# Performance work log

Hardware: AMD Instinct MI355X
Metric: run time of the kernel (lower is better)

Reference implementation:

```python
import jax, jax.numpy as jnp
import numpy as np

EMBED_DIM = 1024
VOCAB = 32000
B, S = 4, 4096


def setup_inputs() -> dict:
    key = jax.random.key(0)
    ks = jax.random.split(key, 6)
    scale = 1.0 / np.sqrt(EMBED_DIM)
    x = jax.random.randint(ks[0], (B, S), 0, VOCAB, dtype=jnp.int64)
    embed = jax.random.normal(ks[1], (VOCAB, EMBED_DIM), dtype=jnp.float32)
    qkv_w = jax.random.normal(ks[2], (EMBED_DIM, 3 * EMBED_DIM), dtype=jnp.float32) * scale
    qkv_b = jnp.zeros((3 * EMBED_DIM,), dtype=jnp.float32)
    out_w = jax.random.normal(ks[3], (EMBED_DIM, VOCAB), dtype=jnp.float32) * scale
    out_b = jnp.zeros((VOCAB,), dtype=jnp.float32)
    return {"x": x, "embed": embed, "qkv_w": qkv_w, "qkv_b": qkv_b,
            "out_w": out_w, "out_b": out_b}


def reference(x, embed, qkv_w, qkv_b, out_w, out_b):
    h = embed[x]                                   # [B,S,D] token embedding lookup
    qkv = h @ qkv_w + qkv_b                        # [B,S,3D]
    qkv = qkv.reshape(B, S, 3, EMBED_DIM)
    q, k, v = qkv[:, :, 0], qkv[:, :, 1], qkv[:, :, 2]
    logits = jnp.einsum('bqd,bkd->bqk', q, k) / jnp.sqrt(jnp.float32(EMBED_DIM))
    attn = jax.nn.softmax(logits, axis=-1)         # [B,S,S] full score matrix (as in source)
    out = jnp.einsum('bqk,bkd->bqd', attn, v)
    h = out + h                                    # residual
    # source applies output projection then slices last token; equivalent to
    # projecting the last-token hidden only.
    return h[:, -1, :] @ out_w + out_b             # [B, vocab]
```

## Files before the change

### kernel.cpp

```cpp
#include <hip/hip_runtime.h>
#include <hip/hip_bf16.h>

typedef __bf16 bf16;
typedef __bf16 bf16x4 __attribute__((ext_vector_type(4)));
typedef __bf16 bf16x8 __attribute__((ext_vector_type(8)));
typedef float floatx4 __attribute__((ext_vector_type(4)));

#define EMBED 1024
#define VOCAB 32000
#define BB    4
#define SS    4096
#define NTOK  (BB * SS)
#define NKV   2048
#define NSEG  16

__device__ __forceinline__ void async_copy16(void* lds, const void* g) {
    __builtin_amdgcn_global_load_lds(
        (const __attribute__((address_space(1))) unsigned int*)g,
        (__attribute__((address_space(3))) unsigned int*)lds, 16, 0, 0);
}

__global__ void gather_embed(const int* __restrict__ x,
                             const float* __restrict__ embed,
                             bf16* __restrict__ h,
                             float* __restrict__ h_last,
                             float* __restrict__ h_final) {
    int t = blockIdx.x;
    int tid = threadIdx.x;
    int row = x[t];
    const float4* src = (const float4*)(embed + (size_t)row * EMBED);
    float4 v = src[tid];
    bf16x4 o; o.x = (bf16)v.x; o.y = (bf16)v.y; o.z = (bf16)v.z; o.w = (bf16)v.w;
    *(bf16x4*)(h + (size_t)t * EMBED + tid * 4) = o;
    if ((t & (SS - 1)) == SS - 1) {
        int b = t >> 12;
        *(float4*)(h_last  + b * EMBED + tid * 4) = v;
        *(float4*)(h_final + b * EMBED + tid * 4) = v;
    }
}

__global__ void wkvt_transpose(const float* __restrict__ qkv_w,
                               bf16* __restrict__ WkvT) {
    __shared__ float T[32][33];
    int n0 = blockIdx.x * 32, d0 = blockIdx.y * 32;
    int tid = threadIdx.x;
    int c = tid & 31, r = tid >> 5;
#pragma unroll
    for (int i = 0; i < 4; ++i) {
        int d = r + i * 8;
        T[c][d] = qkv_w[(size_t)(d0 + d) * (3 * EMBED) + EMBED + n0 + c];
    }
    __syncthreads();
#pragma unroll
    for (int i = 0; i < 4; ++i) {
        int n = r + i * 8;
        WkvT[(size_t)(n0 + n) * EMBED + d0 + c] = (bf16)T[n][c];
    }
}

__global__ void q_gemm(const float* __restrict__ h_last,
                       const float* __restrict__ qkv_w,
                       float* __restrict__ qpart) {
    __shared__ float hs[BB * 64];
    int tid = threadIdx.x;
    int seg = blockIdx.x, d0 = seg * 64;
    hs[tid] = h_last[(tid >> 6) * EMBED + d0 + (tid & 63)];
    __syncthreads();
    int j0 = tid * 4;
    floatx4 acc[BB];
#pragma unroll
    for (int b = 0; b < BB; ++b) acc[b] = (floatx4)0.0f;
#pragma unroll 4
    for (int dd = 0; dd < 64; ++dd) {
        float4 w = *(const float4*)(qkv_w + (size_t)(d0 + dd) * (3 * EMBED) + j0);
#pragma unroll
        for (int b = 0; b < BB; ++b) {
            float hv = hs[b * 64 + dd];
            acc[b][0] += hv * w.x; acc[b][1] += hv * w.y;
            acc[b][2] += hv * w.z; acc[b][3] += hv * w.w;
        }
    }
#pragma unroll
    for (int b = 0; b < BB; ++b)
        *(floatx4*)(qpart + ((size_t)seg * BB + b) * EMBED + j0) = acc[b];
}

__global__ void q_reduce(const float* __restrict__ qpart,
                         const float* __restrict__ qkv_b,
                         float* __restrict__ q) {
    int k = blockIdx.x * 256 + threadIdx.x;
    int b = k >> 10, d = k & (EMBED - 1);
    float s = qkv_b[d];
#pragma unroll
    for (int sg = 0; sg < NSEG; ++sg) s += qpart[((size_t)sg * BB + b) * EMBED + d];
    q[k] = s;
}

__global__ __launch_bounds__(256, 2) void gemm_kv(
    const bf16* __restrict__ A,
    const bf16* __restrict__ BT,
    const float* __restrict__ bias,
    bf16* __restrict__ C) {
    __shared__ bf16 As[128 * 32];
    __shared__ bf16 Bs[128 * 32];
    const int K = EMBED;
    int tid = threadIdx.x;
    int wave = tid >> 6, lane = tid & 63;
    int wm = wave >> 1, wn = wave & 1;
    int quad = lane >> 4, l16 = lane & 15;

    floatx4 acc[4][4];
#pragma unroll
    for (int a = 0; a < 4; ++a)
#pragma unroll
        for (int b = 0; b < 4; ++b) acc[a][b] = (floatx4)0.0f;

    const bf16* Abase = A + (size_t)blockIdx.x * 128 * K;
    const bf16* Bbase = BT + (size_t)blockIdx.y * 128 * K;

    for (int k0 = 0; k0 < K; k0 += 32) {
        __syncthreads();
#pragma unroll
        for (int i = 0; i < 2; ++i) {
            int c = wave * 128 + i * 64 + lane;
            int row = c >> 2, ko = (c & 3) * 8;
            async_copy16(As + c * 8, Abase + (size_t)row * K + k0 + ko);
            async_copy16(Bs + c * 8, Bbase + (size_t)row * K + k0 + ko);
        }
        __syncthreads();
        bf16x8 af[4], bfr[4];
#pragma unroll
        for (int mt = 0; mt < 4; ++mt)
            af[mt] = *(const bf16x8*)(As + (wm * 64 + mt * 16 + l16) * 32 + quad * 8);
#pragma unroll
        for (int nt = 0; nt < 4; ++nt)
            bfr[nt] = *(const bf16x8*)(Bs + (wn * 64 + nt * 16 + l16) * 32 + quad * 8);
#pragma unroll
        for (int mt = 0; mt < 4; ++mt)
#pragma unroll
            for (int nt = 0; nt < 4; ++nt)
                acc[mt][nt] = __builtin_amdgcn_mfma_f32_16x16x32_bf16(
                    af[mt], bfr[nt], acc[mt][nt], 0, 0, 0);
    }

    int crow0 = blockIdx.x * 128 + wm * 64;
    int ccol0 = blockIdx.y * 128 + wn * 64;
#pragma unroll
    for (int mt = 0; mt < 4; ++mt)
#pragma unroll
        for (int nt = 0; nt < 4; ++nt) {
            int col = ccol0 + nt * 16 + l16;
            float bs = bias[col];
#pragma unroll
            for (int r = 0; r < 4; ++r) {
                int row = crow0 + mt * 16 + quad * 4 + r;
                C[(size_t)row * NKV + col] = (bf16)(acc[mt][nt][r] + bs);
            }
        }
}

__global__ void attn_logits(const bf16* __restrict__ KV,
                            const float* __restrict__ q,
                            float* __restrict__ logits) {
    __shared__ float qs[EMBED];
    int b = blockIdx.x >> 10;
    int t = (blockIdx.x & 1023) * 4 + (threadIdx.x >> 6);
    int lane = threadIdx.x & 63;
    *(float4*)(qs + threadIdx.x * 4) = *(const float4*)(q + b * EMBED + threadIdx.x * 4);
    __syncthreads();
    const bf16* Krow = KV + (size_t)(b * SS + t) * NKV;
    float sum = 0.0f;
#pragma unroll
    for (int i = 0; i < 2; ++i) {
        int d0 = i * 512 + lane * 8;
        bf16x8 kv8 = *(const bf16x8*)(Krow + d0);
        float4 qa = *(const float4*)(qs + d0);
        float4 qc = *(const float4*)(qs + d0 + 4);
        sum += qa.x * (float)kv8[0] + qa.y * (float)kv8[1] +
               qa.z * (float)kv8[2] + qa.w * (float)kv8[3] +
               qc.x * (float)kv8[4] + qc.y * (float)kv8[5] +
               qc.z * (float)kv8[6] + qc.w * (float)kv8[7];
    }
#pragma unroll
    for (int o = 32; o; o >>= 1) sum += __shfl_down(sum, o);
    if (lane == 0) logits[b * SS + t] = sum * 0.03125f;
}

__global__ void softmax_k(const float* __restrict__ logits,
                          float* __restrict__ wts) {
    int b = blockIdx.x, tid = threadIdx.x;
    __shared__ float redm[16], reds[16];
    const float* l = logits + b * SS;
    float x0 = l[tid], x1 = l[tid + 1024], x2 = l[tid + 2048], x3 = l[tid + 3072];
    float m = fmaxf(fmaxf(x0, x1), fmaxf(x2, x3));
#pragma unroll
    for (int o = 32; o; o >>= 1) m = fmaxf(m, __shfl_down(m, o));
    if ((tid & 63) == 0) redm[tid >> 6] = m;
    __syncthreads();
    float M = redm[0];
#pragma unroll
    for (int i = 1; i < 16; ++i) M = fmaxf(M, redm[i]);
    float e0 = expf(x0 - M), e1 = expf(x1 - M), e2 = expf(x2 - M), e3 = expf(x3 - M);
    float s = e0 + e1 + e2 + e3;
#pragma unroll
    for (int o = 32; o; o >>= 1) s += __shfl_down(s, o);
    if ((tid & 63) == 0) reds[tid >> 6] = s;
    __syncthreads();
    float S = 0.0f;
#pragma unroll
    for (int i = 0; i < 16; ++i) S += reds[i];
    float inv = 1.0f / S;
    float* w = wts + b * SS;
    w[tid] = e0 * inv; w[tid + 1024] = e1 * inv;
    w[tid + 2048] = e2 * inv; w[tid + 3072] = e3 * inv;
}

__global__ void attn_av(const bf16* __restrict__ KV,
                        const float* __restrict__ wts,
                        float* __restrict__ h_final) {
    int b = blockIdx.x >> 6, ts = blockIdx.x & 63;
    int tid = threadIdx.x;
    __shared__ float wsh[64];
    if (tid < 64) wsh[tid] = wts[b * SS + ts * 64 + tid];
    __syncthreads();
    int d = tid * 4;
    const bf16* Vb = KV + (size_t)(b * SS + ts * 64) * NKV + EMBED + d;
    float a0 = 0, a1 = 0, a2 = 0, a3 = 0;
#pragma unroll 4
    for (int j = 0; j < 64; ++j) {
        bf16x4 v = *(const bf16x4*)(Vb + (size_t)j * NKV);
        float w = wsh[j];
        a0 += w * (float)v.x; a1 += w * (float)v.y;
        a2 += w * (float)v.z; a3 += w * (float)v.w;
    }
    atomicAdd(h_final + b * EMBED + d + 0, a0);
    atomicAdd(h_final + b * EMBED + d + 1, a1);
    atomicAdd(h_final + b * EMBED + d + 2, a2);
    atomicAdd(h_final + b * EMBED + d + 3, a3);
}

__global__ void out_gemm(const float* __restrict__ h_final,
                         const float* __restrict__ out_w,
                         float* __restrict__ opart) {
    __shared__ float hs[BB * 64];
    int tid = threadIdx.x;
    int seg = blockIdx.y, d0 = seg * 64;
    hs[tid] = h_final[(tid >> 6) * EMBED + d0 + (tid & 63)];
    __syncthreads();
    int j0 = blockIdx.x * 1024 + tid * 4;
    if (j0 >= VOCAB) return;
    floatx4 acc[BB];
#pragma unroll
    for (int b = 0; b < BB; ++b) acc[b] = (floatx4)0.0f;
#pragma unroll 4
    for (int dd = 0; dd < 64; ++dd) {
        float4 w = *(const float4*)(out_w + (size_t)(d0 + dd) * VOCAB + j0);
#pragma unroll
        for (int b = 0; b < BB; ++b) {
            float hv = hs[b * 64 + dd];
            acc[b][0] += hv * w.x; acc[b][1] += hv * w.y;
            acc[b][2] += hv * w.z; acc[b][3] += hv * w.w;
        }
    }
#pragma unroll
    for (int b = 0; b < BB; ++b)
        *(floatx4*)(opart + ((size_t)seg * BB + b) * VOCAB + j0) = acc[b];
}

__global__ void out_reduce(const float* __restrict__ opart,
                           const float* __restrict__ out_b,
                           float* __restrict__ out) {
    int i = blockIdx.x * 256 + threadIdx.x;
    if (i >= BB * VOCAB) return;
    int b = i / VOCAB, j = i - b * VOCAB;
    float s = out_b[j];
#pragma unroll
    for (int sg = 0; sg < NSEG; ++sg) s += opart[((size_t)sg * BB + b) * VOCAB + j];
    out[i] = s;
}

extern "C" void kernel_launch(void* const* d_in, const int* in_sizes, int n_in,
                              void* d_out, int out_size, void* d_ws, size_t ws_size,
                              hipStream_t stream) {
    const int*   x      = (const int*)d_in[0];
    const float* embed  = (const float*)d_in[1];
    const float* qkv_w  = (const float*)d_in[2];
    const float* qkv_b  = (const float*)d_in[3];
    const float* out_w  = (const float*)d_in[4];
    const float* out_b  = (const float*)d_in[5];
    float* out = (float*)d_out;

    char* ws = (char*)d_ws;
    bf16*  h       = (bf16*)(ws);
    float* opart   = (float*)(ws);
    bf16*  KV      = (bf16*)(ws + 33554432);
    bf16*  WkvT    = (bf16*)(ws + 100663296);
    float* h_last  = (float*)(ws + 104857600);
    float* h_final = (float*)(ws + 104873984);
    float* q       = (float*)(ws + 104890368);
    float* logits  = (float*)(ws + 104906752);
    float* wts     = (float*)(ws + 104972288);
    float* qpart   = (float*)(ws + 105037824);

    gather_embed<<<NTOK, 256, 0, stream>>>(x, embed, h, h_last, h_final);
    wkvt_transpose<<<dim3(64, 32), 256, 0, stream>>>(qkv_w, WkvT);
    q_gemm<<<NSEG, 256, 0, stream>>>(h_last, qkv_w, qpart);
    q_reduce<<<16, 256, 0, stream>>>(qpart, qkv_b, q);
    gemm_kv<<<dim3(NTOK / 128, NKV / 128), 256, 0, stream>>>(
        h, WkvT, qkv_b + EMBED, KV);
    attn_logits<<<SS, 256, 0, stream>>>(KV, q, logits);
    softmax_k<<<BB, 1024, 0, stream>>>(logits, wts);
    attn_av<<<256, 256, 0, stream>>>(KV, wts, h_final);
    out_gemm<<<dim3(32, NSEG), 256, 0, stream>>>(h_final, out_w, opart);
    out_reduce<<<(BB * VOCAB + 255) / 256, 256, 0, stream>>>(opart, out_b, out);
}
```

Baseline: 397.3 us.

## Fuse prep kernels, flash-style split attention, fused q projection, wider out_gemm

Merges the embedding gather and weight transpose into one launch and handles four tokens per block. The q projection becomes a single kernel without a partial-sum reduce. Logits, softmax and AV are replaced by a chunked online-softmax pass plus a combine kernel, which removes the intermediate logits/weights buffers and the atomics. out_gemm now computes eight columns per thread. Together these cut launch count and global round-trips, at the cost of a small q kernel that runs on only 32 blocks and a serial inner loop over 512 weights per thread.

New measurement: 418.1 us. 1.05x slower.

```diff
diff --git a/kernel.cpp b/kernel.cpp
--- a/kernel.cpp
+++ b/kernel.cpp
@@ -13,6 +13,8 @@
 #define NTOK  (BB * SS)
 #define NKV   2048
 #define NSEG  16
+#define TCH   32
+#define NCH   (SS / TCH)
 
 __device__ __forceinline__ void async_copy16(void* lds, const void* g) {
     __builtin_amdgcn_global_load_lds(
@@ -20,80 +22,71 @@
         (__attribute__((address_space(3))) unsigned int*)lds, 16, 0, 0);
 }
 
-__global__ void gather_embed(const int* __restrict__ x,
-                             const float* __restrict__ embed,
-                             bf16* __restrict__ h,
-                             float* __restrict__ h_last,
-                             float* __restrict__ h_final) {
-    int t = blockIdx.x;
+__global__ void prep(const int* __restrict__ x,
+                     const float* __restrict__ embed,
+                     const float* __restrict__ qkv_w,
+                     bf16* __restrict__ h,
+                     float* __restrict__ h_last,
+                     bf16* __restrict__ WkvT) {
+    __shared__ float T[32 * 33];
+    int bid = blockIdx.x, tid = threadIdx.x;
+    if (bid < NTOK / 4) {
+        int t0 = bid * 4;
+        int r0 = x[t0], r1 = x[t0 + 1], r2 = x[t0 + 2], r3 = x[t0 + 3];
+        float4 v0 = *(const float4*)(embed + (size_t)r0 * EMBED + tid * 4);
+        float4 v1 = *(const float4*)(embed + (size_t)r1 * EMBED + tid * 4);
+        float4 v2 = *(const float4*)(embed + (size_t)r2 * EMBED + tid * 4);
+        float4 v3 = *(const float4*)(embed + (size_t)r3 * EMBED + tid * 4);
+        bf16x4 o0, o1, o2, o3;
+        o0.x=(bf16)v0.x; o0.y=(bf16)v0.y; o0.z=(bf16)v0.z; o0.w=(bf16)v0.w;
+        o1.x=(bf16)v1.x; o1.y=(bf16)v1.y; o1.z=(bf16)v1.z; o1.w=(bf16)v1.w;
+        o2.x=(bf16)v2.x; o2.y=(bf16)v2.y; o2.z=(bf16)v2.z; o2.w=(bf16)v2.w;
+        o3.x=(bf16)v3.x; o3.y=(bf16)v3.y; o3.z=(bf16)v3.z; o3.w=(bf16)v3.w;
+        *(bf16x4*)(h + (size_t)(t0 + 0) * EMBED + tid * 4) = o0;
+        *(bf16x4*)(h + (size_t)(t0 + 1) * EMBED + tid * 4) = o1;
+        *(bf16x4*)(h + (size_t)(t0 + 2) * EMBED + tid * 4) = o2;
+        *(bf16x4*)(h + (size_t)(t0 + 3) * EMBED + tid * 4) = o3;
+        if ((bid & 1023) == 1023) {
+            int b = bid >> 10;
+            *(float4*)(h_last + b * EMBED + tid * 4) = v3;
+        }
+    } else {
+        int bw = bid - NTOK / 4;
+        int n0 = (bw & 63) * 32, d0 = (bw >> 6) * 32;
+        int c = tid & 31, r = tid >> 5;
+#pragma unroll
+        for (int i = 0; i < 4; ++i) {
+            int d = r + i * 8;
+            T[c * 33 + d] = qkv_w[(size_t)(d0 + d) * (3 * EMBED) + EMBED + n0 + c];
+        }
+        __syncthreads();
+#pragma unroll
+        for (int i = 0; i < 4; ++i) {
+            int n = r + i * 8;
+            WkvT[(size_t)(n0 + n) * EMBED + d0 + c] = (bf16)T[n * 33 + c];
+        }
+    }
+}
+
+__global__ void q_fused(const float* __restrict__ h_last,
+                        const float* __restrict__ qkv_w,
+                        const float* __restrict__ qkv_b,
+                        float* __restrict__ q) {
+    __shared__ float hs[BB * EMBED];
     int tid = threadIdx.x;
-    int row = x[t];
-    const float4* src = (const float4*)(embed + (size_t)row * EMBED);
-    float4 v = src[tid];
-    bf16x4 o; o.x = (bf16)v.x; o.y = (bf16)v.y; o.z = (bf16)v.z; o.w = (bf16)v.w;
-    *(bf16x4*)(h + (size_t)t * EMBED + tid * 4) = o;
-    if ((t & (SS - 1)) == SS - 1) {
-        int b = t >> 12;
-        *(float4*)(h_last  + b * EMBED + tid * 4) = v;
-        *(float4*)(h_final + b * EMBED + tid * 4) = v;
-    }
-}
-
-__global__ void wkvt_transpose(const float* __restrict__ qkv_w,
-                               bf16* __restrict__ WkvT) {
-    __shared__ float T[32][33];
-    int n0 = blockIdx.x * 32, d0 = blockIdx.y * 32;
-    int tid = threadIdx.x;
-    int c = tid & 31, r = tid >> 5;
-#pragma unroll
-    for (int i = 0; i < 4; ++i) {
-        int d = r + i * 8;
-        T[c][d] = qkv_w[(size_t)(d0 + d) * (3 * EMBED) + EMBED + n0 + c];
-    }
-    __syncthreads();
-#pragma unroll
-    for (int i = 0; i < 4; ++i) {
-        int n = r + i * 8;
-        WkvT[(size_t)(n0 + n) * EMBED + d0 + c] = (bf16)T[n][c];
-    }
-}
-
-__global__ void q_gemm(const float* __restrict__ h_last,
-                       const float* __restrict__ qkv_w,
-                       float* __restrict__ qpart) {
-    __shared__ float hs[BB * 64];
-    int tid = threadIdx.x;
-    int seg = blockIdx.x, d0 = seg * 64;
-    hs[tid] = h_last[(tid >> 6) * EMBED + d0 + (tid & 63)];
-    __syncthreads();
-    int j0 = tid * 4;
-    floatx4 acc[BB];
-#pragma unroll
-    for (int b = 0; b < BB; ++b) acc[b] = (floatx4)0.0f;
-#pragma unroll 4
-    for (int dd = 0; dd < 64; ++dd) {
-        float4 w = *(const float4*)(qkv_w + (size_t)(d0 + dd) * (3 * EMBED) + j0);
-#pragma unroll
-        for (int b = 0; b < BB; ++b) {
-            float hv = hs[b * 64 + dd];
-            acc[b][0] += hv * w.x; acc[b][1] += hv * w.y;
-            acc[b][2] += hv * w.z; acc[b][3] += hv * w.w;
-        }
-    }
-#pragma unroll
-    for (int b = 0; b < BB; ++b)
-        *(floatx4*)(qpart + ((size_t)seg * BB + b) * EMBED + j0) = acc[b];
-}
-
-__global__ void q_reduce(const float* __restrict__ qpart,
-                         const float* __restrict__ qkv_b,
-                         float* __restrict__ q) {
-    int k = blockIdx.x * 256 + threadIdx.x;
-    int b = k >> 10, d = k & (EMBED - 1);
-    float s = qkv_b[d];
-#pragma unroll
-    for (int sg = 0; sg < NSEG; ++sg) s += qpart[((size_t)sg * BB + b) * EMBED + d];
-    q[k] = s;
+    for (int i = tid; i < BB * EMBED / 4; i += 256)
+        *(float4*)(hs + i * 4) = *(const float4*)(h_last + i * 4);
+    __syncthreads();
+    int w = tid >> 6, lane = tid & 63;
+    int j = blockIdx.x * 32 + (lane & 31);
+    int dh = lane >> 5;
+    const float* hb = hs + w * EMBED + dh * 512;
+    float acc = 0.0f;
+#pragma unroll 8
+    for (int d = 0; d < 512; ++d)
+        acc += hb[d] * qkv_w[(size_t)(dh * 512 + d) * (3 * EMBED) + j];
+    acc += __shfl_down(acc, 32);
+    if (lane < 32) q[w * EMBED + j] = acc + qkv_b[j];
 }
 
 __global__ __launch_bounds__(256, 2) void gemm_kv(
@@ -159,84 +152,110 @@
         }
 }
 
-__global__ void attn_logits(const bf16* __restrict__ KV,
-                            const float* __restrict__ q,
-                            float* __restrict__ logits) {
+__global__ __launch_bounds__(256) void attn_partial(
+    const bf16* __restrict__ KV,
+    const float* __restrict__ q,
+    float* __restrict__ pacc,
+    float* __restrict__ pms) {
     __shared__ float qs[EMBED];
-    int b = blockIdx.x >> 10;
-    int t = (blockIdx.x & 1023) * 4 + (threadIdx.x >> 6);
-    int lane = threadIdx.x & 63;
-    *(float4*)(qs + threadIdx.x * 4) = *(const float4*)(q + b * EMBED + threadIdx.x * 4);
-    __syncthreads();
-    const bf16* Krow = KV + (size_t)(b * SS + t) * NKV;
-    float sum = 0.0f;
-#pragma unroll
-    for (int i = 0; i < 2; ++i) {
-        int d0 = i * 512 + lane * 8;
-        bf16x8 kv8 = *(const bf16x8*)(Krow + d0);
-        float4 qa = *(const float4*)(qs + d0);
-        float4 qc = *(const float4*)(qs + d0 + 4);
-        sum += qa.x * (float)kv8[0] + qa.y * (float)kv8[1] +
-               qa.z * (float)kv8[2] + qa.w * (float)kv8[3] +
-               qc.x * (float)kv8[4] + qc.y * (float)kv8[5] +
-               qc.z * (float)kv8[6] + qc.w * (float)kv8[7];
-    }
-#pragma unroll
-    for (int o = 32; o; o >>= 1) sum += __shfl_down(sum, o);
-    if (lane == 0) logits[b * SS + t] = sum * 0.03125f;
-}
-
-__global__ void softmax_k(const float* __restrict__ logits,
-                          float* __restrict__ wts) {
-    int b = blockIdx.x, tid = threadIdx.x;
-    __shared__ float redm[16], reds[16];
-    const float* l = logits + b * SS;
-    float x0 = l[tid], x1 = l[tid + 1024], x2 = l[tid + 2048], x3 = l[tid + 3072];
-    float m = fmaxf(fmaxf(x0, x1), fmaxf(x2, x3));
-#pragma unroll
-    for (int o = 32; o; o >>= 1) m = fmaxf(m, __shfl_down(m, o));
-    if ((tid & 63) == 0) redm[tid >> 6] = m;
-    __syncthreads();
-    float M = redm[0];
-#pragma unroll
-    for (int i = 1; i < 16; ++i) M = fmaxf(M, redm[i]);
-    float e0 = expf(x0 - M), e1 = expf(x1 - M), e2 = expf(x2 - M), e3 = expf(x3 - M);
-    float s = e0 + e1 + e2 + e3;
-#pragma unroll
-    for (int o = 32; o; o >>= 1) s += __shfl_down(s, o);
-    if ((tid & 63) == 0) reds[tid >> 6] = s;
-    __syncthreads();
-    float S = 0.0f;
-#pragma unroll
-    for (int i = 0; i < 16; ++i) S += reds[i];
-    float inv = 1.0f / S;
-    float* w = wts + b * SS;
-    w[tid] = e0 * inv; w[tid + 1024] = e1 * inv;
-    w[tid + 2048] = e2 * inv; w[tid + 3072] = e3 * inv;
-}
-
-__global__ void attn_av(const bf16* __restrict__ KV,
-                        const float* __restrict__ wts,
-                        float* __restrict__ h_final) {
-    int b = blockIdx.x >> 6, ts = blockIdx.x & 63;
-    int tid = threadIdx.x;
-    __shared__ float wsh[64];
-    if (tid < 64) wsh[tid] = wts[b * SS + ts * 64 + tid];
-    __syncthreads();
-    int d = tid * 4;
-    const bf16* Vb = KV + (size_t)(b * SS + ts * 64) * NKV + EMBED + d;
+    __shared__ float lg[TCH];
+    __shared__ float wt[TCH];
+    int bid = blockIdx.x;
+    int b = bid >> 7, ch = bid & (NCH - 1);
+    int t0 = ch * TCH;
+    int tid = threadIdx.x, w = tid >> 6, lane = tid & 63;
+    *(float4*)(qs + tid * 4) = *(const float4*)(q + b * EMBED + tid * 4);
+    __syncthreads();
+    for (int j = 0; j < 8; ++j) {
+        int tl = w * 8 + j;
+        const bf16* Krow = KV + (size_t)(b * SS + t0 + tl) * NKV;
+        float sum = 0.0f;
+#pragma unroll
+        for (int i = 0; i < 2; ++i) {
+            int d0 = i * 512 + lane * 8;
+            bf16x8 k8 = *(const bf16x8*)(Krow + d0);
+            float4 qa = *(const float4*)(qs + d0);
+            float4 qc = *(const float4*)(qs + d0 + 4);
+            sum += qa.x * (float)k8[0] + qa.y * (float)k8[1] +
+                   qa.z * (float)k8[2] + qa.w * (float)k8[3] +
+                   qc.x * (float)k8[4] + qc.y * (float)k8[5] +
+                   qc.z * (float)k8[6] + qc.w * (float)k8[7];
+        }
+#pragma unroll
+        for (int o = 32; o; o >>= 1) sum += __shfl_down(sum, o);
+        if (lane == 0) lg[tl] = sum * 0.03125f;
+    }
+    __syncthreads();
+    float m = -1e30f;
+#pragma unroll
+    for (int i = 0; i < TCH; ++i) m = fmaxf(m, lg[i]);
+    if (tid < TCH) wt[tid] = expf(lg[tid] - m);
+    __syncthreads();
+    float ssum = 0.0f;
+#pragma unroll
+    for (int i = 0; i < TCH; ++i) ssum += wt[i];
+    int d4 = tid * 4;
+    const bf16* Vb = KV + (size_t)(b * SS + t0) * NKV + EMBED + d4;
     float a0 = 0, a1 = 0, a2 = 0, a3 = 0;
 #pragma unroll 4
-    for (int j = 0; j < 64; ++j) {
-        bf16x4 v = *(const bf16x4*)(Vb + (size_t)j * NKV);
-        float w = wsh[j];
-        a0 += w * (float)v.x; a1 += w * (float)v.y;
-        a2 += w * (float)v.z; a3 += w * (float)v.w;
-    }
-    atomicAdd(h_final + b * EMBED + d + 0, a0);
-    atomicAdd(h_final + b * EMBED + d + 1, a1);
-    atomicAdd(h_final + b * EMBED + d + 2, a2);
-    atomicAdd(h_final + b * EMBED + d + 3, a3);
+    for (int t = 0; t < TCH; ++t) {
+        bf16x4 v = *(const bf16x4*)(Vb + (size_t)t * NKV);
+        float wv = wt[t];
+        a0 += wv * (float)v.x; a1 += wv * (float)v.y;
+        a2 += wv * (float)v.z; a3 += wv * (float)v.w;
+    }
+    float* pa = pacc + (size_t)(b * NCH + ch) * EMBED + d4;
+    pa[0] = a0; pa[1] = a1; pa[2] = a2; pa[3] = a3;
+    if (tid == 0) {
+        pms[(b * NCH + ch) * 2 + 0] = m;
+        pms[(b * NCH + ch) * 2 + 1] = ssum;
+    }
+}
+
+__global__ void attn_combine(const float* __restrict__ pacc,
+                             const float* __restrict__ pms,
+                             const float* __restrict__ h_last,
+                             float* __restrict__ h_final) {
+    __shared__ float pmL[NCH], psL[NCH], eL[NCH];
+    __shared__ float red[8][32][4];
+    int b = blockIdx.x >> 3, g = blockIdx.x & 7;
+    int tid = threadIdx.x;
+    if (tid < NCH) {
+        pmL[tid] = pms[(b * NCH + tid) * 2 + 0];
+        psL[tid] = pms[(b * NCH + tid) * 2 + 1];
+    }
+    __syncthreads();
+    float M = -1e30f;
+#pragma unroll 8
+    for (int i = 0; i < NCH; ++i) M = fmaxf(M, pmL[i]);
+    if (tid < NCH) eL[tid] = expf(pmL[tid] - M);
+    __syncthreads();
+    float S = 0.0f;
+#pragma unroll 8
+    for (int i = 0; i < NCH; ++i) S += psL[i] * eL[i];
+    int dq = tid & 31, tg = tid >> 5;
+    int d4 = g * 128 + dq * 4;
+    float a0 = 0, a1 = 0, a2 = 0, a3 = 0;
+    for (int ts = tg * 16; ts < tg * 16 + 16; ++ts) {
+        float e = eL[ts];
+        const float* p = pacc + (size_t)(b * NCH + ts) * EMBED + d4;
+        a0 += e * p[0]; a1 += e * p[1]; a2 += e * p[2]; a3 += e * p[3];
+    }
+    red[tg][dq][0] = a0; red[tg][dq][1] = a1;
+    red[tg][dq][2] = a2; red[tg][dq][3] = a3;
+    __syncthreads();
+    if (tg == 0) {
+#pragma unroll
+        for (int i = 1; i < 8; ++i) {
+            a0 += red[i][dq][0]; a1 += red[i][dq][1];
+            a2 += red[i][dq][2]; a3 += red[i][dq][3];
+        }
+        float inv = 1.0f / S;
+        const float* r = h_last + b * EMBED + d4;
+        float* o = h_final + b * EMBED + d4;
+        o[0] = r[0] + a0 * inv; o[1] = r[1] + a1 * inv;
+        o[2] = r[2] + a2 * inv; o[3] = r[3] + a3 * inv;
+    }
 }
 
 __global__ void out_gemm(const float* __restrict__ h_final,
@@ -247,24 +266,31 @@
     int seg = blockIdx.y, d0 = seg * 64;
     hs[tid] = h_final[(tid >> 6) * EMBED + d0 + (tid & 63)];
     __syncthreads();
-    int j0 = blockIdx.x * 1024 + tid * 4;
+    int j0 = blockIdx.x * 2048 + tid * 8;
     if (j0 >= VOCAB) return;
-    floatx4 acc[BB];
-#pragma unroll
-    for (int b = 0; b < BB; ++b) acc[b] = (floatx4)0.0f;
-#pragma unroll 4
+    floatx4 aL[BB], aH[BB];
+#pragma unroll
+    for (int b = 0; b < BB; ++b) { aL[b] = (floatx4)0.0f; aH[b] = (floatx4)0.0f; }
+#pragma unroll 2
     for (int dd = 0; dd < 64; ++dd) {
-        float4 w = *(const float4*)(out_w + (size_t)(d0 + dd) * VOCAB + j0);
+        const float* wr = out_w + (size_t)(d0 + dd) * VOCAB + j0;
+        float4 w0 = *(const float4*)wr;
+        float4 w1 = *(const float4*)(wr + 4);
 #pragma unroll
         for (int b = 0; b < BB; ++b) {
             float hv = hs[b * 64 + dd];
-            acc[b][0] += hv * w.x; acc[b][1] += hv * w.y;
-            acc[b][2] += hv * w.z; acc[b][3] += hv * w.w;
-        }
-    }
-#pragma unroll
-    for (int b = 0; b < BB; ++b)
-        *(floatx4*)(opart + ((size_t)seg * BB + b) * VOCAB + j0) = acc[b];
+            aL[b][0] += hv * w0.x; aL[b][1] += hv * w0.y;
+            aL[b][2] += hv * w0.z; aL[b][3] += hv * w0.w;
+            aH[b][0] += hv * w1.x; aH[b][1] += hv * w1.y;
+            aH[b][2] += hv * w1.z; aH[b][3] += hv * w1.w;
+        }
+    }
+#pragma unroll
+    for (int b = 0; b < BB; ++b) {
+        float* op = opart + ((size_t)seg * BB + b) * VOCAB + j0;
+        *(floatx4*)op = aL[b];
+        *(floatx4*)(op + 4) = aH[b];
+    }
 }
 
 __global__ void out_reduce(const float* __restrict__ opart,
@@ -293,24 +319,20 @@
     char* ws = (char*)d_ws;
     bf16*  h       = (bf16*)(ws);
     float* opart   = (float*)(ws);
+    float* pacc    = (float*)(ws + 16777216);
+    float* pms     = (float*)(ws + 20971520);
     bf16*  KV      = (bf16*)(ws + 33554432);
     bf16*  WkvT    = (bf16*)(ws + 100663296);
     float* h_last  = (float*)(ws + 104857600);
     float* h_final = (float*)(ws + 104873984);
     float* q       = (float*)(ws + 104890368);
-    float* logits  = (float*)(ws + 104906752);
-    float* wts     = (float*)(ws + 104972288);
-    float* qpart   = (float*)(ws + 105037824);
-
-    gather_embed<<<NTOK, 256, 0, stream>>>(x, embed, h, h_last, h_final);
-    wkvt_transpose<<<dim3(64, 32), 256, 0, stream>>>(qkv_w, WkvT);
-    q_gemm<<<NSEG, 256, 0, stream>>>(h_last, qkv_w, qpart);
-    q_reduce<<<16, 256, 0, stream>>>(qpart, qkv_b, q);
+
+    prep<<<NTOK / 4 + 2048, 256, 0, stream>>>(x, embed, qkv_w, h, h_last, WkvT);
+    q_fused<<<32, 256, 0, stream>>>(h_last, qkv_w, qkv_b, q);
     gemm_kv<<<dim3(NTOK / 128, NKV / 128), 256, 0, stream>>>(
         h, WkvT, qkv_b + EMBED, KV);
-    attn_logits<<<SS, 256, 0, stream>>>(KV, q, logits);
-    softmax_k<<<BB, 1024, 0, stream>>>(logits, wts);
-    attn_av<<<256, 256, 0, stream>>>(KV, wts, h_final);
-    out_gemm<<<dim3(32, NSEG), 256, 0, stream>>>(h_final, out_w, opart);
+    attn_partial<<<BB * NCH, 256, 0, stream>>>(KV, q, pacc, pms);
+    attn_combine<<<32, 256, 0, stream>>>(pacc, pms, h_last, h_final);
+    out_gemm<<<dim3(16, NSEG), 256, 0, stream>>>(h_final, out_w, opart);
     out_reduce<<<(BB * VOCAB + 255) / 256, 256, 0, stream>>>(opart, out_b, out);
 }
```
